# Optimization experiments

Hardware: AMD Instinct MI355X
Metric: run time of the kernel (lower is better)

The kernel has to match this reference:

```python
import jax, jax.numpy as jnp
import numpy as np

B, C, H, W = 4, 256, 64, 64
C8 = C // 8


def setup_inputs() -> dict:
    key = jax.random.key(0)
    ks = jax.random.split(key, 10)
    return {
        "x": jax.random.normal(ks[0], (B, C, H, W), jnp.float32),
        "x_encoder": jax.random.normal(ks[1], (B, C, H, W), jnp.float32),
        "Wq": jax.random.normal(ks[2], (C8, C), jnp.float32) * 0.05,
        "bq": jax.random.normal(ks[3], (C8,), jnp.float32) * 0.05,
        "Wk": jax.random.normal(ks[4], (C8, C), jnp.float32) * 0.05,
        "bk": jax.random.normal(ks[5], (C8,), jnp.float32) * 0.05,
        "Wv": jax.random.normal(ks[6], (C, C), jnp.float32) * 0.05,
        "bv": jax.random.normal(ks[7], (C,), jnp.float32) * 0.05,
        "h_pos": jax.random.normal(ks[8], (1, C8, H, 1), jnp.float32),
        "w_pos": jax.random.normal(ks[9], (1, C8, 1, W), jnp.float32),
        "gamma": jnp.zeros((1,), jnp.float32),
    }


def reference(x, x_encoder, Wq, bq, Wk, bk, Wv, bv, h_pos, w_pos, gamma):
    b, c, h, w = x.shape
    n = h * w
    c8 = Wq.shape[0]
    # 1x1 convs are channel-wise matmuls over flattened spatial dim
    xf = x.reshape(b, c, n)            # [B, C, N]
    xe = x_encoder.reshape(b, c, n)    # [B, C, N]
    q = jnp.einsum("oc,bcn->bno", Wq, xf) + bq[None, None, :]   # [B, N, C8]
    k = jnp.einsum("oc,bcn->bon", Wk, xe) + bk[None, :, None]   # [B, C8, N]
    energy = jnp.einsum("bnc,bcm->bnm", q, k)                    # [B, N, N]
    pos = (h_pos + w_pos).reshape(c8, n)                         # [C8, N]
    energy = energy + jnp.einsum("bnc,cm->bnm", q, pos)
    attn = jax.nn.softmax(energy, axis=-1)                       # [B, N, N]
    v = jnp.einsum("oc,bcn->bon", Wv, xe) + bv[None, :, None]    # [B, C, N]
    out = jnp.einsum("bcm,bnm->bcn", v, attn).reshape(b, c, h, w)
    return gamma * out + x
```

## Files before the change

kernel.cpp:

```cpp
#include <hip/hip_runtime.h>
#include <hip/hip_bf16.h>
#include <math.h>

#define BB 4
#define CC 256
#define C8 32
#define HH 64
#define WW 64
#define NN 4096
#define QBLK 64
#define NT 32
#define LOG2E 1.44269504088896340736f

typedef __attribute__((ext_vector_type(8)))  short bh8;
typedef __attribute__((ext_vector_type(4)))  float f4;
typedef __attribute__((ext_vector_type(16))) float f16v;

#if __has_builtin(__builtin_amdgcn_exp2f)
#define EXP2(x) __builtin_amdgcn_exp2f(x)
#else
#define EXP2(x) exp2f(x)
#endif

static __device__ __forceinline__ unsigned short f2bf(float f) {
    union { float f; unsigned int u; } v; v.f = f;
    return (unsigned short)((v.u + 0x7FFFu + ((v.u >> 16) & 1u)) >> 16);
}

static __device__ __forceinline__ unsigned int cvtpk(float lo, float hi) {
    unsigned int r;
    asm("v_cvt_pk_bf16_f32 %0, %1, %2" : "=v"(r) : "v"(lo), "v"(hi));
    return r;
}

static __device__ __forceinline__ bh8 pack_frag(unsigned int w0, unsigned int w1,
                                                unsigned int w2, unsigned int w3) {
    union { unsigned int u[4]; bh8 v; } z;
    z.u[0] = w0; z.u[1] = w1; z.u[2] = w2; z.u[3] = w3;
    return z.v;
}

__global__ __launch_bounds__(256) void wconv_kernel(
    const float* __restrict__ Wq, const float* __restrict__ Wk,
    const float* __restrict__ Wv, unsigned short* __restrict__ wb)
{
    int f = (blockIdx.x * 256 + threadIdx.x) * 4;
    const float* src;
    if (f < 32 * 256)           src = Wq + f;
    else if (f < 64 * 256)      src = Wk + (f - 32 * 256);
    else                        src = Wv + (f - 64 * 256);
    float4 v = *reinterpret_cast<const float4*>(src);
    ushort4 o;
    o.x = f2bf(v.x); o.y = f2bf(v.y); o.z = f2bf(v.z); o.w = f2bf(v.w);
    *reinterpret_cast<ushort4*>(wb + f) = o;
}

__global__ __launch_bounds__(640, 1) void proj_kernel(
    const float* __restrict__ x, const float* __restrict__ xe,
    const unsigned short* __restrict__ wb,
    const float* __restrict__ bq, const float* __restrict__ bk,
    const float* __restrict__ bv,
    const float* __restrict__ hp, const float* __restrict__ wp,
    unsigned short* __restrict__ qb, unsigned short* __restrict__ kb,
    unsigned short* __restrict__ vv)
{
    const int b  = blockIdx.x & 3;
    const int n0 = (blockIdx.x >> 2) << 6;
    const int t  = threadIdx.x;
    const int w  = t >> 6;
    const int lane = t & 63;
    const int l15 = lane & 15, l4 = lane >> 4;

    __shared__ unsigned short xT[64][256];
    __shared__ unsigned short xeT[64][256];

    bh8 af[2][8];
    {
        const unsigned short* wrow = wb + (size_t)(w * 32 + l15) * 256 + l4 * 8;
        #pragma unroll
        for (int kk = 0; kk < 8; ++kk) {
            af[0][kk] = *reinterpret_cast<const bh8*>(wrow + kk * 32);
            af[1][kk] = *reinterpret_cast<const bh8*>(wrow + 16 * 256 + kk * 32);
        }
    }

    {
        const float* xb  = x  + (size_t)(b * CC) * NN + n0;
        const float* xeb = xe + (size_t)(b * CC) * NN + n0;
        for (int i = t; i < 4096; i += 640) {
            int c = i >> 4, n4 = (i & 15) << 2;
            float4 a = *reinterpret_cast<const float4*>(xb  + (size_t)c * NN + n4);
            float4 e = *reinterpret_cast<const float4*>(xeb + (size_t)c * NN + n4);
            #pragma unroll
            for (int j = 0; j < 4; ++j) {
                int n  = n4 + j;
                int cs = c ^ ((n & 7) << 3);
                xT[n][cs]  = f2bf((&a.x)[j]);
                xeT[n][cs] = f2bf((&e.x)[j]);
            }
        }
    }
    __syncthreads();

    const unsigned short* lds = (w == 0) ? &xT[0][0] : &xeT[0][0];
    f4 acc[2][4] = {};
    #pragma unroll
    for (int kk = 0; kk < 8; ++kk) {
        bh8 bf[4];
        #pragma unroll
        for (int nf = 0; nf < 4; ++nf) {
            int n  = nf * 16 + l15;
            int c0 = (kk * 32 + l4 * 8) ^ ((n & 7) << 3);
            bf[nf] = *reinterpret_cast<const bh8*>(lds + n * 256 + c0);
        }
        #pragma unroll
        for (int nf = 0; nf < 4; ++nf) {
            acc[0][nf] = __builtin_amdgcn_mfma_f32_16x16x32_bf16(af[0][kk], bf[nf], acc[0][nf], 0, 0, 0);
            acc[1][nf] = __builtin_amdgcn_mfma_f32_16x16x32_bf16(af[1][kk], bf[nf], acc[1][nf], 0, 0, 0);
        }
    }

    if (w < 2) {
        unsigned short* dst = (w == 0 ? qb : kb) + (size_t)(b * NN) * C8;
        const float* bias = (w == 0) ? bq : bk;
        #pragma unroll
        for (int mf = 0; mf < 2; ++mf) {
            #pragma unroll
            for (int nf = 0; nf < 4; ++nf) {
                int n  = n0 + nf * 16 + l15;
                int oo = mf * 16 + l4 * 4;
                ushort4 pk;
                #pragma unroll
                for (int r = 0; r < 4; ++r) {
                    int o = oo + r;
                    float val = acc[mf][nf][r] + bias[o];
                    if (w == 1) val += hp[o * HH + (n >> 6)] + wp[o * WW + (n & 63)];
                    else        val *= LOG2E;
                    (&pk.x)[r] = f2bf(val);
                }
                *reinterpret_cast<ushort4*>(dst + (size_t)n * C8 + oo) = pk;
            }
        }
    } else {
        #pragma unroll
        for (int mf = 0; mf < 2; ++mf) {
            int cb = (w - 2) * 32 + mf * 16 + l4 * 4;
            #pragma unroll
            for (int r = 0; r < 4; ++r) {
                float bvv = bv[cb + r];
                #pragma unroll
                for (int nf = 0; nf < 4; ++nf) {
                    int n = n0 + nf * 16 + l15;
                    size_t idx = (((size_t)b * 128 + (n >> 5)) * 256 + cb + r) * 32 + (n & 31);
                    vv[idx] = f2bf(acc[mf][nf][r] + bvv);
                }
            }
        }
    }
}

__global__ __launch_bounds__(512, 1) void attn_flash_kernel(
    const unsigned short* __restrict__ qb, const unsigned short* __restrict__ kb,
    const unsigned short* __restrict__ v,  const float* __restrict__ x,
    const float* __restrict__ gamma, float* __restrict__ out)
{
    const int b    = blockIdx.x & 3;
    const int r0   = (blockIdx.x >> 2) << 6;
    const int t    = threadIdx.x;
    const int w    = t >> 6;
    const int lane = t & 63;
    const int l31  = lane & 31;
    const int h    = lane >> 5;
    const int ks   = w & 3;
    const int cq   = w >> 2;
    const int c0   = cq * 128;

    __shared__ float mO[2][3][64][17];
    __shared__ float mML[2][3][64];

    bh8 qf[2][2];
    #pragma unroll
    for (int qt = 0; qt < 2; ++qt)
        #pragma unroll
        for (int cf = 0; cf < 2; ++cf)
            qf[qt][cf] = *reinterpret_cast<const bh8*>(
                qb + ((size_t)(b * NN) + r0 + qt * 32 + l31) * C8 + cf * 16 + 8 * h);

    const int kb0 = ks * (NN / 4);
    const unsigned short* kp = kb + ((size_t)(b * NN) + kb0 + l31) * C8 + 8 * h;
    const unsigned short* vbase =
        v + (((size_t)b * 128 + ks * 32) * 256 + c0 + l31) * 32 + 8 * h;

    f16v zero16;
    #pragma unroll
    for (int r = 0; r < 16; ++r) zero16[r] = 0.f;

    f16v acc[2][4];
    #pragma unroll
    for (int qt = 0; qt < 2; ++qt)
        #pragma unroll
        for (int ct = 0; ct < 4; ++ct)
            acc[qt][ct] = zero16;

    float l_[2] = { 0.f, 0.f };

    bh8 vf[4][2], kf0, kf1;
    #pragma unroll
    for (int ct = 0; ct < 4; ++ct)
        #pragma unroll
        for (int kk = 0; kk < 2; ++kk)
            vf[ct][kk] = *reinterpret_cast<const bh8*>(vbase + ct * 1024 + kk * 16);
    kf0 = *reinterpret_cast<const bh8*>(kp);
    kf1 = *reinterpret_cast<const bh8*>(kp + 16);

    for (int tt = 0; tt < NT; ++tt) {
        const int tn = (tt + 1 < NT) ? tt + 1 : tt;
        bh8 nk0, nk1;
        {
            const unsigned short* knx = kp + (size_t)tn * 32 * C8;
            nk0 = *reinterpret_cast<const bh8*>(knx);
            nk1 = *reinterpret_cast<const bh8*>(knx + 16);
        }

        f16v s0 = __builtin_amdgcn_mfma_f32_32x32x16_bf16(kf0, qf[0][0], zero16, 0, 0, 0);
        s0 = __builtin_amdgcn_mfma_f32_32x32x16_bf16(kf1, qf[0][1], s0, 0, 0, 0);
        f16v s1 = __builtin_amdgcn_mfma_f32_32x32x16_bf16(kf0, qf[1][0], zero16, 0, 0, 0);
        s1 = __builtin_amdgcn_mfma_f32_32x32x16_bf16(kf1, qf[1][1], s1, 0, 0, 0);
        kf0 = nk0; kf1 = nk1;

        #pragma unroll
        for (int qt = 0; qt < 2; ++qt) {
            f16v s = qt ? s1 : s0;
            #pragma unroll
            for (int r = 0; r < 16; ++r) s[r] = EXP2(s[r]);
            float rs = (((s[0] + s[1]) + (s[2] + s[3])) + ((s[4] + s[5]) + (s[6] + s[7])))
                     + (((s[8] + s[9]) + (s[10] + s[11])) + ((s[12] + s[13]) + (s[14] + s[15])));
            l_[qt] += rs;

            bh8 pf[2];
            #pragma unroll
            for (int kk = 0; kk < 2; ++kk) {
                unsigned int A  = cvtpk(s[8 * kk + 0], s[8 * kk + 1]);
                unsigned int A2 = cvtpk(s[8 * kk + 2], s[8 * kk + 3]);
                unsigned int Bv = cvtpk(s[8 * kk + 4], s[8 * kk + 5]);
                unsigned int B2 = cvtpk(s[8 * kk + 6], s[8 * kk + 7]);
                asm volatile("v_permlane32_swap_b32 %0, %1" : "+v"(Bv), "+v"(A));
                asm volatile("v_permlane32_swap_b32 %0, %1" : "+v"(B2), "+v"(A2));
                pf[kk] = pack_frag(A, A2, Bv, B2);
            }

            __builtin_amdgcn_s_setprio(1);
            #pragma unroll
            for (int ct = 0; ct < 4; ++ct) {
                acc[qt][ct] = __builtin_amdgcn_mfma_f32_32x32x16_bf16(vf[ct][0], pf[0], acc[qt][ct], 0, 0, 0);
                acc[qt][ct] = __builtin_amdgcn_mfma_f32_32x32x16_bf16(vf[ct][1], pf[1], acc[qt][ct], 0, 0, 0);
            }
            __builtin_amdgcn_s_setprio(0);
        }

        {
            const unsigned short* vt = vbase + (size_t)tn * 8192;
            #pragma unroll
            for (int ct = 0; ct < 4; ++ct)
                #pragma unroll
                for (int kk = 0; kk < 2; ++kk)
                    vf[ct][kk] = *reinterpret_cast<const bh8*>(vt + ct * 1024 + kk * 16);
        }
    }

    float lt[2];
    #pragma unroll
    for (int qt = 0; qt < 2; ++qt) {
        float u0 = l_[qt], u1 = l_[qt];
        asm volatile("v_permlane32_swap_b32 %0, %1" : "+v"(u0), "+v"(u1));
        lt[qt] = u0 + u1;
    }

    const float gg = gamma[0];
    #pragma unroll
    for (int qt = 0; qt < 2; ++qt) {
        float Linv = 0.f;
        #pragma unroll
        for (int ct = 0; ct < 4; ++ct) {
            if (ks != 0) {
                #pragma unroll
                for (int rq = 0; rq < 4; ++rq) {
                    f4 tv;
                    tv[0] = acc[qt][ct][rq * 4 + 0];
                    tv[1] = acc[qt][ct][rq * 4 + 1];
                    tv[2] = acc[qt][ct][rq * 4 + 2];
                    tv[3] = acc[qt][ct][rq * 4 + 3];
                    *reinterpret_cast<f4*>(&mO[cq][ks - 1][lane][rq * 4]) = tv;
                }
                if (ct == 0) mML[cq][ks - 1][lane] = lt[qt];
            }
            __syncthreads();
            if (ks == 0) {
                if (ct == 0) {
                    float L = lt[qt] + mML[cq][0][lane] + mML[cq][1][lane] + mML[cq][2][lane];
                    Linv = gg / L;
                }
                #pragma unroll
                for (int r = 0; r < 16; ++r) {
                    float o = acc[qt][ct][r] + mO[cq][0][lane][r]
                            + mO[cq][1][lane][r] + mO[cq][2][lane][r];
                    int c = c0 + ct * 32 + (r & 3) + 8 * (r >> 2) + 4 * h;
                    size_t idx = ((size_t)(b * CC) + c) * NN + r0 + qt * 32 + l31;
                    out[idx] = o * Linv + x[idx];
                }
            }
            __syncthreads();
        }
    }
}

extern "C" void kernel_launch(void* const* d_in, const int* in_sizes, int n_in,
                              void* d_out, int out_size, void* d_ws, size_t ws_size,
                              hipStream_t stream)
{
    (void)in_sizes; (void)n_in; (void)out_size; (void)ws_size;

    const float* x   = (const float*)d_in[0];
    const float* xe  = (const float*)d_in[1];
    const float* Wq  = (const float*)d_in[2];
    const float* bq  = (const float*)d_in[3];
    const float* Wk  = (const float*)d_in[4];
    const float* bk  = (const float*)d_in[5];
    const float* Wv  = (const float*)d_in[6];
    const float* bv  = (const float*)d_in[7];
    const float* hp  = (const float*)d_in[8];
    const float* wp  = (const float*)d_in[9];
    const float* gam = (const float*)d_in[10];
    float* out = (float*)d_out;

    char* ws = (char*)d_ws;
    unsigned short* qb = (unsigned short*)ws;
    unsigned short* kb = (unsigned short*)(ws + (size_t)BB * NN * C8 * 2);
    unsigned short* v  = (unsigned short*)(ws + 2 * (size_t)BB * NN * C8 * 2);
    unsigned short* wbuf = (unsigned short*)(ws + 2 * (size_t)BB * NN * C8 * 2
                                                + (size_t)BB * CC * NN * 2);

    wconv_kernel<<<80, 256, 0, stream>>>(Wq, Wk, Wv, wbuf);
    proj_kernel<<<BB * (NN / 64), 640, 0, stream>>>(x, xe, wbuf, bq, bk, bv, hp, wp, qb, kb, v);
    attn_flash_kernel<<<BB * (NN / QBLK), 512, 0, stream>>>(qb, kb, v, x, gam, out);
}
```

Measured before the change: 83.35 us.

## Fuse weight bf16 conversion into projection kernel and interleave score MFMAs

Removes the separate weight-conversion kernel launch; the projection kernel now reads fp32 weights directly and converts them to bf16 fragments with packed convert instructions. In the attention loop, each query tile's score MFMAs are computed inside the per-tile loop instead of both up front, which lowers live registers and lets exp work overlap the other tile's MFMAs. Costs: every projection block rereads fp32 weights (twice the bytes), and the order of the score computations changes.

```diff
diff --git a/kernel.cpp b/kernel.cpp
--- a/kernel.cpp
+++ b/kernel.cpp
@@ -40,24 +40,10 @@
     return z.v;
 }
 
-__global__ __launch_bounds__(256) void wconv_kernel(
-    const float* __restrict__ Wq, const float* __restrict__ Wk,
-    const float* __restrict__ Wv, unsigned short* __restrict__ wb)
-{
-    int f = (blockIdx.x * 256 + threadIdx.x) * 4;
-    const float* src;
-    if (f < 32 * 256)           src = Wq + f;
-    else if (f < 64 * 256)      src = Wk + (f - 32 * 256);
-    else                        src = Wv + (f - 64 * 256);
-    float4 v = *reinterpret_cast<const float4*>(src);
-    ushort4 o;
-    o.x = f2bf(v.x); o.y = f2bf(v.y); o.z = f2bf(v.z); o.w = f2bf(v.w);
-    *reinterpret_cast<ushort4*>(wb + f) = o;
-}
-
 __global__ __launch_bounds__(640, 1) void proj_kernel(
     const float* __restrict__ x, const float* __restrict__ xe,
-    const unsigned short* __restrict__ wb,
+    const float* __restrict__ Wq, const float* __restrict__ Wk,
+    const float* __restrict__ Wv,
     const float* __restrict__ bq, const float* __restrict__ bk,
     const float* __restrict__ bv,
     const float* __restrict__ hp, const float* __restrict__ wp,
@@ -76,11 +62,17 @@
 
     bh8 af[2][8];
     {
-        const unsigned short* wrow = wb + (size_t)(w * 32 + l15) * 256 + l4 * 8;
-        #pragma unroll
-        for (int kk = 0; kk < 8; ++kk) {
-            af[0][kk] = *reinterpret_cast<const bh8*>(wrow + kk * 32);
-            af[1][kk] = *reinterpret_cast<const bh8*>(wrow + 16 * 256 + kk * 32);
+        const float* wr0 = (w == 0) ? Wq : (w == 1 ? Wk : Wv + (size_t)(w - 2) * 32 * CC);
+        #pragma unroll
+        for (int mh = 0; mh < 2; ++mh) {
+            const float* rp = wr0 + (size_t)(mh * 16 + l15) * CC + l4 * 8;
+            #pragma unroll
+            for (int kk = 0; kk < 8; ++kk) {
+                float4 a = *reinterpret_cast<const float4*>(rp + kk * 32);
+                float4 c = *reinterpret_cast<const float4*>(rp + kk * 32 + 4);
+                af[mh][kk] = pack_frag(cvtpk(a.x, a.y), cvtpk(a.z, a.w),
+                                       cvtpk(c.x, c.y), cvtpk(c.z, c.w));
+            }
         }
     }
 
@@ -222,15 +214,11 @@
             nk1 = *reinterpret_cast<const bh8*>(knx + 16);
         }
 
-        f16v s0 = __builtin_amdgcn_mfma_f32_32x32x16_bf16(kf0, qf[0][0], zero16, 0, 0, 0);
-        s0 = __builtin_amdgcn_mfma_f32_32x32x16_bf16(kf1, qf[0][1], s0, 0, 0, 0);
-        f16v s1 = __builtin_amdgcn_mfma_f32_32x32x16_bf16(kf0, qf[1][0], zero16, 0, 0, 0);
-        s1 = __builtin_amdgcn_mfma_f32_32x32x16_bf16(kf1, qf[1][1], s1, 0, 0, 0);
-        kf0 = nk0; kf1 = nk1;
-
         #pragma unroll
         for (int qt = 0; qt < 2; ++qt) {
-            f16v s = qt ? s1 : s0;
+            f16v s = __builtin_amdgcn_mfma_f32_32x32x16_bf16(kf0, qf[qt][0], zero16, 0, 0, 0);
+            s = __builtin_amdgcn_mfma_f32_32x32x16_bf16(kf1, qf[qt][1], s, 0, 0, 0);
+
             #pragma unroll
             for (int r = 0; r < 16; ++r) s[r] = EXP2(s[r]);
             float rs = (((s[0] + s[1]) + (s[2] + s[3])) + ((s[4] + s[5]) + (s[6] + s[7])))
@@ -266,6 +254,7 @@
                 for (int kk = 0; kk < 2; ++kk)
                     vf[ct][kk] = *reinterpret_cast<const bh8*>(vt + ct * 1024 + kk * 16);
         }
+        kf0 = nk0; kf1 = nk1;
     }
 
     float lt[2];
@@ -337,10 +326,7 @@
     unsigned short* qb = (unsigned short*)ws;
     unsigned short* kb = (unsigned short*)(ws + (size_t)BB * NN * C8 * 2);
     unsigned short* v  = (unsigned short*)(ws + 2 * (size_t)BB * NN * C8 * 2);
-    unsigned short* wbuf = (unsigned short*)(ws + 2 * (size_t)BB * NN * C8 * 2
-                                                + (size_t)BB * CC * NN * 2);
-
-    wconv_kernel<<<80, 256, 0, stream>>>(Wq, Wk, Wv, wbuf);
-    proj_kernel<<<BB * (NN / 64), 640, 0, stream>>>(x, xe, wbuf, bq, bk, bv, hp, wp, qb, kb, v);
+
+    proj_kernel<<<BB * (NN / 64), 640, 0, stream>>>(x, xe, Wq, Wk, Wv, bq, bk, bv, hp, wp, qb, kb, v);
     attn_flash_kernel<<<BB * (NN / QBLK), 512, 0, stream>>>(qb, kb, v, x, gam, out);
 }
```

Result: slower. 85.41 us, median of 2 (+2.5%).
